# Kernel optimization log

Hardware: AMD Instinct MI355X
Metric: run time of the kernel (lower is better)

Reference implementation:

```python
import jax, jax.numpy as jnp
import numpy as np

B, V, S, T_IN, STEP, W, M = 4, 2, 256, 10, 5, 32, 16
NB = 6  # number of FNO2d blocks


def gelu(x):
    return jax.nn.gelu(x, approximate=False)  # torch F.gelu default = exact erf


def conv1(x, w, b):
    # 1x1x1 Conv3d: x (B,Cin,V,S,S), w (Cout,Cin), b (Cout,)
    return jnp.einsum('oc,bcvxy->bovxy', w, x) + b[None, :, None, None, None]


def spectral_conv(x, w1, w2):
    # x: (B,W,V,S,S) real; w1,w2: (W,W,V,M,M) complex64
    x_ft = jnp.fft.rfft2(x)  # (B,W,V,S,S//2+1) complex64
    o1 = jnp.einsum('bivxy,iovxy->bovxy', x_ft[..., :M, :M], w1)
    o2 = jnp.einsum('bivxy,iovxy->bovxy', x_ft[..., S - M:, :M], w2)
    F = S // 2 + 1
    out_ft = jnp.zeros((x.shape[0], W, V, S, F), jnp.complex64)
    out_ft = out_ft.at[..., :M, :M].set(o1).at[..., S - M:, :M].set(o2)
    return jnp.fft.irfft2(out_ft, s=(S, S))


def setup_inputs() -> dict:
    key = jax.random.key(0)
    ks = jax.random.split(key, 24)
    rn = lambda k, shp, s=0.05: jax.random.normal(k, shp, jnp.float32) * s
    sc = 1.0 / W  # torch init: scale * rand
    d = {}
    d['x'] = jax.random.normal(ks[0], (B, V, S, S, T_IN), jnp.float32)
    d['fc0_w'] = rn(ks[1], (T_IN + 2, W))
    d['fc0_b'] = rn(ks[2], (W,))
    d['w1r'] = jax.random.uniform(ks[3], (NB, W, W, V, M, M), jnp.float32) * sc
    d['w1i'] = jax.random.uniform(ks[4], (NB, W, W, V, M, M), jnp.float32) * sc
    d['w2r'] = jax.random.uniform(ks[5], (NB, W, W, V, M, M), jnp.float32) * sc
    d['w2i'] = jax.random.uniform(ks[6], (NB, W, W, V, M, M), jnp.float32) * sc
    d['mlp1_w'] = rn(ks[7], (NB, W, W))
    d['mlp1_b'] = rn(ks[8], (NB, W))
    d['mlp2_w'] = rn(ks[9], (NB, W, W))
    d['mlp2_b'] = rn(ks[10], (NB, W))
    d['ww'] = rn(ks[11], (NB, W, W))
    d['wb'] = rn(ks[12], (NB, W))
    d['bw'] = rn(ks[13], (NB, W, 2))
    d['bb'] = rn(ks[14], (NB, W))
    d['fc1_w'] = rn(ks[15], (W, 256))
    d['fc1_b'] = rn(ks[16], (256,))
    d['fc2_w'] = rn(ks[17], (256, STEP))
    d['fc2_b'] = rn(ks[18], (STEP,))
    return d


def reference(x, fc0_w, fc0_b, w1r, w1i, w2r, w2i, mlp1_w, mlp1_b, mlp2_w, mlp2_b,
              ww, wb, bw, bb, fc1_w, fc1_b, fc2_w, fc2_b):
    Bn = x.shape[0]
    gx = jnp.linspace(9.5, 10.5, S, dtype=jnp.float32)
    gy = jnp.linspace(-0.5, 0.5, S, dtype=jnp.float32)
    grid2 = jnp.stack([jnp.broadcast_to(gx[:, None], (S, S)),
                       jnp.broadcast_to(gy[None, :], (S, S))], 0)  # (2,S,S)
    grid = jnp.broadcast_to(grid2[None, :, None], (Bn, 2, V, S, S))  # (B,2,V,S,S)

    h = jnp.concatenate([x, jnp.transpose(grid, (0, 2, 3, 4, 1))], axis=-1)  # (B,V,S,S,T_IN+2)
    h = h @ fc0_w + fc0_b
    h = jnp.transpose(h, (0, 4, 1, 2, 3))  # (B,W,V,S,S)

    def block(i, h):
        x1 = spectral_conv(h, w1r[i] + 1j * w1i[i], w2r[i] + 1j * w2i[i])
        x1 = conv1(gelu(conv1(x1, mlp1_w[i], mlp1_b[i])), mlp2_w[i], mlp2_b[i])
        x2 = conv1(h, ww[i], wb[i])
        x3 = conv1(grid, bw[i], bb[i])
        return gelu(x1 + x2 + x3)

    x0 = block(0, h)
    h = block(1, x0)
    h = block(2, h) + x0
    x1s = block(3, h)
    h = block(4, x1s)
    h = block(5, h) + x1s

    h = jnp.transpose(h, (0, 2, 3, 4, 1))  # (B,V,S,S,W)
    h = gelu(h @ fc1_w + fc1_b)
    return h @ fc2_w + fc2_b  # (B,V,S,S,STEP)
```

## Files before the change

### kernel.cpp

```cpp
#include <hip/hip_runtime.h>

#define kB 4
#define kV 2
#define kS 256
#define kW 32
#define kM 16
#define kNB 6
#define kTIN 10
#define kSTEP 5

#define NPLANE 65536
#define NBWV   (kB*kW*kV)
#define BIGN   (kB*kW*kV*NPLANE)
#define CHS    (kV*NPLANE)

#define OFF_BIG0 0
#define OFF_BIG1 16777216
#define OFF_BIG2 33554432
#define OFF_FXR  52428800
#define OFF_FXI  52559872
#define OFF_GR   52690944
#define OFF_GI   52822016
#define OFF_TIC  52969472
#define OFF_TIS  52977664
#define OFF_IYC  52985856
#define OFF_IYS  52989952
#define OFF_WHI  52994048
#define OFF_WLO  52998144
#define OFF_YAH  53002240
#define OFF_YAL  53006336
#define OFF_XBH  53010432
#define OFF_XBL  53022720
#define OFF_M2H  53035008
#define OFF_M2L  53038080
#define OFF_WWH  53041152
#define OFF_WWL  53044224

typedef short bf16x8 __attribute__((ext_vector_type(8)));
typedef float f32x4 __attribute__((ext_vector_type(4)));

__device__ __forceinline__ unsigned short bf16_rne(float f){
    union { float f; unsigned int u; } x; x.f = f;
    unsigned int u = x.u + 0x7fffu + ((x.u>>16)&1u);
    return (unsigned short)(u>>16);
}
__device__ __forceinline__ float bf16_tof(unsigned short h){
    union { unsigned int u; float f; } x; x.u = ((unsigned int)h)<<16;
    return x.f;
}

__device__ __forceinline__ float gelu_f(float x){
    float z = fabsf(x) * 0.70710678118654752f;
    float t = __builtin_amdgcn_rcpf(1.0f + 0.3275911f*z);
    float poly = t*(0.254829592f + t*(-0.284496736f + t*(1.421413741f + t*(-1.453152027f + t*1.061405429f))));
    float e = __expf(-z*z);
    float erf_abs = 1.0f - poly*e;
    float ph = (x >= 0.0f) ? (1.0f + erf_abs) : (1.0f - erf_abs);
    return 0.5f * x * ph;
}

__global__ void k_tables(float* ws, const float* __restrict__ fc1w,
                         const float* __restrict__ m2w, const float* __restrict__ wwv){
    const double PI = 3.14159265358979323846;
    int t = blockIdx.x*256 + threadIdx.x;
    if (t < 8192){
        int j2 = t>>8, x2 = t&255;
        int kx2 = (j2<16) ? j2 : (224+j2);
        int p2 = (kx2*x2)&255;
        double a2 = (double)p2*(PI/128.0);
        ws[OFF_TIC+t] = (float)cos(a2);
        ws[OFF_TIS+t] = (float)sin(a2);
    }
    if (t < 4096){
        int k = t>>8, y = t&255;
        int p = (k*y)&255;
        double a = (double)p*(PI/128.0);
        float sc = 1.0f/65536.0f;
        ws[OFF_IYC+t] = (k==0 ? 1.0f : 2.0f*(float)cos(a))*sc;
        ws[OFF_IYS+t] = (k==0 ? 0.0f : -2.0f*(float)sin(a))*sc;
    }
    if (t < 1024){
        int nt = t>>6, l = t&63;
        int o = nt*16 + (l&15), c0 = (l>>4)*8;
        unsigned int hw[4], lw[4];
        #pragma unroll
        for (int e2=0; e2<4; e2++){
            float f0 = fc1w[(c0+2*e2  )*256 + o];
            float f1 = fc1w[(c0+2*e2+1)*256 + o];
            unsigned short h0 = bf16_rne(f0), h1 = bf16_rne(f1);
            unsigned short l0 = bf16_rne(f0 - bf16_tof(h0));
            unsigned short l1 = bf16_rne(f1 - bf16_tof(h1));
            hw[e2] = (unsigned int)h0 | ((unsigned int)h1<<16);
            lw[e2] = (unsigned int)l0 | ((unsigned int)l1<<16);
        }
        unsigned int* whi = (unsigned int*)(ws+OFF_WHI);
        unsigned int* wlo = (unsigned int*)(ws+OFF_WLO);
        #pragma unroll
        for (int e2=0; e2<4; e2++){
            whi[t*4+e2] = hw[e2];
            wlo[t*4+e2] = lw[e2];
        }
    }
    if (t < 1024){
        int mt = t>>9, kt = (t>>6)&7, l = t&63;
        int ky = l&15;
        unsigned int* yah = (unsigned int*)(ws+OFF_YAH);
        unsigned int* yal = (unsigned int*)(ws+OFF_YAL);
        #pragma unroll
        for (int e2=0; e2<4; e2++){
            int y0 = kt*32 + (l>>4)*8 + 2*e2;
            double a0 = (double)((ky*y0)&255)*(PI/128.0);
            double a1 = (double)((ky*(y0+1))&255)*(PI/128.0);
            float v0 = (mt==0) ? (float)cos(a0) : -(float)sin(a0);
            float v1 = (mt==0) ? (float)cos(a1) : -(float)sin(a1);
            unsigned short h0 = bf16_rne(v0), h1 = bf16_rne(v1);
            unsigned short s0 = bf16_rne(v0 - bf16_tof(h0));
            unsigned short s1 = bf16_rne(v1 - bf16_tof(h1));
            yah[t*4+e2] = (unsigned int)h0 | ((unsigned int)h1<<16);
            yal[t*4+e2] = (unsigned int)s0 | ((unsigned int)s1<<16);
        }
    }
    if (t < 3072){
        int tab = t>>10, jh = (t>>9)&1, kt = (t>>6)&7, l = t&63;
        int j = jh*16 + (l&15);
        int kx = (j<16) ? j : (224+j);
        unsigned int* xbh = (unsigned int*)(ws+OFF_XBH);
        unsigned int* xbl = (unsigned int*)(ws+OFF_XBL);
        #pragma unroll
        for (int e2=0; e2<4; e2++){
            int x0 = kt*32 + (l>>4)*8 + 2*e2;
            double a0 = (double)((kx*x0)&255)*(PI/128.0);
            double a1 = (double)((kx*(x0+1))&255)*(PI/128.0);
            float v0, v1;
            if (tab==0){ v0=(float)cos(a0); v1=(float)cos(a1); }
            else if (tab==1){ v0=-(float)sin(a0); v1=-(float)sin(a1); }
            else { v0=(float)sin(a0); v1=(float)sin(a1); }
            unsigned short h0 = bf16_rne(v0), h1 = bf16_rne(v1);
            unsigned short s0 = bf16_rne(v0 - bf16_tof(h0));
            unsigned short s1 = bf16_rne(v1 - bf16_tof(h1));
            xbh[t*4+e2] = (unsigned int)h0 | ((unsigned int)h1<<16);
            xbl[t*4+e2] = (unsigned int)s0 | ((unsigned int)s1<<16);
        }
    }
    if (t < 768){
        int blk = t>>7, rem = t&127, mt = rem>>6, l = rem&63;
        int o = mt*16 + (l&15), c0 = (l>>4)*8;
        const float* src = m2w + blk*1024;
        unsigned int* mh = (unsigned int*)(ws+OFF_M2H);
        unsigned int* ml = (unsigned int*)(ws+OFF_M2L);
        #pragma unroll
        for (int e2=0; e2<4; e2++){
            float f0 = src[o*32 + c0+2*e2];
            float f1 = src[o*32 + c0+2*e2+1];
            unsigned short h0 = bf16_rne(f0), h1 = bf16_rne(f1);
            unsigned short s0 = bf16_rne(f0 - bf16_tof(h0));
            unsigned short s1 = bf16_rne(f1 - bf16_tof(h1));
            mh[t*4+e2] = (unsigned int)h0 | ((unsigned int)h1<<16);
            ml[t*4+e2] = (unsigned int)s0 | ((unsigned int)s1<<16);
        }
    }
    if (t >= 768 && t < 1536){
        int t2 = t - 768;
        int blk = t2>>7, rem = t2&127, mt = rem>>6, l = rem&63;
        int o = mt*16 + (l&15), c0 = (l>>4)*8;
        const float* src = wwv + blk*1024;
        unsigned int* mh = (unsigned int*)(ws+OFF_WWH);
        unsigned int* ml = (unsigned int*)(ws+OFF_WWL);
        #pragma unroll
        for (int e2=0; e2<4; e2++){
            float f0 = src[o*32 + c0+2*e2];
            float f1 = src[o*32 + c0+2*e2+1];
            unsigned short h0 = bf16_rne(f0), h1 = bf16_rne(f1);
            unsigned short s0 = bf16_rne(f0 - bf16_tof(h0));
            unsigned short s1 = bf16_rne(f1 - bf16_tof(h1));
            mh[t2*4+e2] = (unsigned int)h0 | ((unsigned int)h1<<16);
            ml[t2*4+e2] = (unsigned int)s0 | ((unsigned int)s1<<16);
        }
    }
}

__global__ void k_fc0(const float* __restrict__ x, const float* __restrict__ w,
                      const float* __restrict__ bias, float* __restrict__ h0){
    int plane = blockIdx.x>>8, xr = blockIdx.x&255, y = threadIdx.x;
    int xy = xr*256+y;
    long p = (long)plane*NPLANE + xy;
    float f[12];
    #pragma unroll
    for (int i=0;i<10;i++) f[i]=x[p*10+i];
    f[10] = 9.5f + xr*(1.0f/255.0f);
    f[11] = -0.5f + y*(1.0f/255.0f);
    float acc[32];
    #pragma unroll
    for (int o=0;o<32;o++) acc[o]=bias[o];
    #pragma unroll
    for (int c=0;c<12;c++){
        float fv=f[c];
        #pragma unroll
        for (int o=0;o<32;o++) acc[o]+=fv*w[c*32+o];
    }
    int b=plane>>1, v=plane&1;
    int base = b*(kW*CHS) + v*NPLANE + xy;
    #pragma unroll
    for (int o=0;o<32;o++) h0[base + o*CHS]=acc[o];
}

__global__ __launch_bounds__(512) void k_fwdfft(const float* __restrict__ h,
        const unsigned int* __restrict__ yah, const unsigned int* __restrict__ yal,
        const unsigned int* __restrict__ xbh, const unsigned int* __restrict__ xbl,
        float* __restrict__ fxr, float* __restrict__ fxi){
    __shared__ float fyrl[16*260], fyil[16*260];
    int bwv = blockIdx.x;
    int tid = threadIdx.x;
    int wv = tid>>6, l = tid&63;

    for (int half=0; half<2; ++half){
        int nt = wv*2 + half;
        int x = nt*16 + (l&15);
        int klo = (l>>4)*8;
        const float* hp = h + bwv*NPLANE + x*256 + klo;
        f32x4 accR = {0.f,0.f,0.f,0.f}, accI = {0.f,0.f,0.f,0.f};
        for (int kt=0; kt<8; ++kt){
            float4 b0 = *reinterpret_cast<const float4*>(hp + kt*32);
            float4 b1 = *reinterpret_cast<const float4*>(hp + kt*32 + 4);
            float bv[8] = {b0.x,b0.y,b0.z,b0.w,b1.x,b1.y,b1.z,b1.w};
            bf16x8 bh, bl;
            #pragma unroll
            for (int e=0;e<8;e++){
                unsigned short hb = bf16_rne(bv[e]);
                bh[e] = (short)hb;
                bl[e] = (short)bf16_rne(bv[e] - bf16_tof(hb));
            }
            uint4 a0h = *reinterpret_cast<const uint4*>(&yah[(kt*64+l)*4]);
            uint4 a0l = *reinterpret_cast<const uint4*>(&yal[(kt*64+l)*4]);
            uint4 a1h = *reinterpret_cast<const uint4*>(&yah[(512 + kt*64 + l)*4]);
            uint4 a1l = *reinterpret_cast<const uint4*>(&yal[(512 + kt*64 + l)*4]);
            bf16x8 AH0 = __builtin_bit_cast(bf16x8, a0h);
            bf16x8 AL0 = __builtin_bit_cast(bf16x8, a0l);
            bf16x8 AH1 = __builtin_bit_cast(bf16x8, a1h);
            bf16x8 AL1 = __builtin_bit_cast(bf16x8, a1l);
            accR = __builtin_amdgcn_mfma_f32_16x16x32_bf16(AH0, bh, accR, 0,0,0);
            accR = __builtin_amdgcn_mfma_f32_16x16x32_bf16(AH0, bl, accR, 0,0,0);
            accR = __builtin_amdgcn_mfma_f32_16x16x32_bf16(AL0, bh, accR, 0,0,0);
            accI = __builtin_amdgcn_mfma_f32_16x16x32_bf16(AH1, bh, accI, 0,0,0);
            accI = __builtin_amdgcn_mfma_f32_16x16x32_bf16(AH1, bl, accI, 0,0,0);
            accI = __builtin_amdgcn_mfma_f32_16x16x32_bf16(AL1, bh, accI, 0,0,0);
        }
        int ky0 = (l>>4)*4;
        #pragma unroll
        for (int r=0;r<4;r++){
            fyrl[(ky0+r)*260 + x] = accR[r];
            fyil[(ky0+r)*260 + x] = accI[r];
        }
    }
    __syncthreads();

    if (wv < 2){
        int jh = wv;
        const float* ar = fyrl + (l&15)*260 + (l>>4)*8;
        const float* ai = fyil + (l&15)*260 + (l>>4)*8;
        f32x4 accR = {0.f,0.f,0.f,0.f}, accI = {0.f,0.f,0.f,0.f};
        for (int kt=0; kt<8; ++kt){
            float4 r0 = *reinterpret_cast<const float4*>(ar + kt*32);
            float4 r1 = *reinterpret_cast<const float4*>(ar + kt*32 + 4);
            float4 i0 = *reinterpret_cast<const float4*>(ai + kt*32);
            float4 i1 = *reinterpret_cast<const float4*>(ai + kt*32 + 4);
            float rv[8] = {r0.x,r0.y,r0.z,r0.w,r1.x,r1.y,r1.z,r1.w};
            float iv[8] = {i0.x,i0.y,i0.z,i0.w,i1.x,i1.y,i1.z,i1.w};
            bf16x8 Rh, Rl, Ih, Il;
            #pragma unroll
            for (int e=0;e<8;e++){
                unsigned short hb = bf16_rne(rv[e]);
                Rh[e] = (short)hb;
                Rl[e] = (short)bf16_rne(rv[e] - bf16_tof(hb));
                unsigned short hb2 = bf16_rne(iv[e]);
                Ih[e] = (short)hb2;
                Il[e] = (short)bf16_rne(iv[e] - bf16_tof(hb2));
            }
            int fb = (jh*512 + kt*64 + l)*4;
            uint4 ch = *reinterpret_cast<const uint4*>(&xbh[fb]);
            uint4 cl = *reinterpret_cast<const uint4*>(&xbl[fb]);
            uint4 sh = *reinterpret_cast<const uint4*>(&xbh[fb + 4096]);
            uint4 sl = *reinterpret_cast<const uint4*>(&xbl[fb + 4096]);
            uint4 ph = *reinterpret_cast<const uint4*>(&xbh[fb + 8192]);
            uint4 pl = *reinterpret_cast<const uint4*>(&xbl[fb + 8192]);
            bf16x8 CH = __builtin_bit_cast(bf16x8, ch);
            bf16x8 CL = __builtin_bit_cast(bf16x8, cl);
            bf16x8 SH = __builtin_bit_cast(bf16x8, sh);
            bf16x8 SL = __builtin_bit_cast(bf16x8, sl);
            bf16x8 PH = __builtin_bit_cast(bf16x8, ph);
            bf16x8 PL = __builtin_bit_cast(bf16x8, pl);
            accR = __builtin_amdgcn_mfma_f32_16x16x32_bf16(Rh, CH, accR, 0,0,0);
            accR = __builtin_amdgcn_mfma_f32_16x16x32_bf16(Rh, CL, accR, 0,0,0);
            accR = __builtin_amdgcn_mfma_f32_16x16x32_bf16(Rl, CH, accR, 0,0,0);
            accR = __builtin_amdgcn_mfma_f32_16x16x32_bf16(Ih, PH, accR, 0,0,0);
            accR = __builtin_amdgcn_mfma_f32_16x16x32_bf16(Ih, PL, accR, 0,0,0);
            accR = __builtin_amdgcn_mfma_f32_16x16x32_bf16(Il, PH, accR, 0,0,0);
            accI = __builtin_amdgcn_mfma_f32_16x16x32_bf16(Rh, SH, accI, 0,0,0);
            accI = __builtin_amdgcn_mfma_f32_16x16x32_bf16(Rh, SL, accI, 0,0,0);
            accI = __builtin_amdgcn_mfma_f32_16x16x32_bf16(Rl, SH, accI, 0,0,0);
            accI = __builtin_amdgcn_mfma_f32_16x16x32_bf16(Ih, CH, accI, 0,0,0);
            accI = __builtin_amdgcn_mfma_f32_16x16x32_bf16(Ih, CL, accI, 0,0,0);
            accI = __builtin_amdgcn_mfma_f32_16x16x32_bf16(Il, CH, accI, 0,0,0);
        }
        int ob = bwv*512 + jh*16 + (l&15);
        int ky0 = (l>>4)*4;
        #pragma unroll
        for (int r=0;r<4;r++){
            fxr[ob + (ky0+r)*32] = accR[r];
            fxi[ob + (ky0+r)*32] = accI[r];
        }
    }
}

__global__ void k_modemix(const float* __restrict__ fxr, const float* __restrict__ fxi,
                          const float* __restrict__ w1r_, const float* __restrict__ w1i_,
                          const float* __restrict__ w2r_, const float* __restrict__ w2i_,
                          const float* __restrict__ m1, float* __restrict__ g2r, float* __restrict__ g2i){
    __shared__ float glr[32*17], gli[32*17];
    int blk = blockIdx.x;
    int jh = blk&1, ky = (blk>>1)&15, v = (blk>>5)&1, b = blk>>6;
    int o = threadIdx.x>>4, jl = threadIdx.x&15;
    int j = jh*16 + jl;
    int kxi = (j<16) ? j : (j-16);
    const float* wr_ = (j<16) ? w1r_ : w2r_;
    const float* wi_ = (j<16) ? w1i_ : w2i_;
    int wbase = (o*kV + v)*256 + kxi*16 + ky;
    int fbase = (b*kW*kV + v)*512 + ky*32 + j;
    float re=0.f, im=0.f;
    #pragma unroll 8
    for (int i=0;i<32;i++){
        float fr=fxr[fbase+i*1024], fi=fxi[fbase+i*1024];
        float wr=wr_[wbase+i*16384], wi=wi_[wbase+i*16384];
        re += fr*wr - fi*wi;
        im += fr*wi + fi*wr;
    }
    glr[o*17+jl]=re; gli[o*17+jl]=im;
    __syncthreads();
    float r2=0.f, i2=0.f;
    #pragma unroll 8
    for (int i=0;i<32;i++){
        float m = m1[o*32+i];
        r2 += m*glr[i*17+jl];
        i2 += m*gli[i*17+jl];
    }
    int gid = ((b*kW + o)*kV + v)*512 + ky*32 + j;
    g2r[gid]=r2; g2i[gid]=i2;
}

__global__ void k_invpoint(const float* __restrict__ g2r, const float* __restrict__ g2i,
                           const float* __restrict__ xic, const float* __restrict__ xis,
                           const float* __restrict__ iyc, const float* __restrict__ iys,
                           const float* __restrict__ b1,
                           const float* h, const float* res, float* out,
                           const unsigned int* __restrict__ m2h, const unsigned int* __restrict__ m2l,
                           const unsigned int* __restrict__ wwh, const unsigned int* __restrict__ wwl,
                           const float* __restrict__ b2,
                           const float* __restrict__ wb_, const float* __restrict__ bw_,
                           const float* __restrict__ bb_){
    __shared__ float frl[16*36], fil[16*36];
    __shared__ float tl[32*260];
    __shared__ float cinit[32], bwy_[32];
    int tid = threadIdx.x;
    int blk = blockIdx.x;
    int b = blk>>9, v = (blk>>8)&1, xr = blk&255;
    float gx = 9.5f + xr*(1.0f/255.0f);
    if (tid < 32){
        cinit[tid] = b2[tid] + wb_[tid] + bb_[tid] + bw_[tid*2]*gx;
        bwy_[tid] = bw_[tid*2+1];
    }

    #pragma unroll
    for (int pp=0; pp<2; pp++){
        int p = tid + pp*256;
        int o = p>>4, k = p&15;
        const float* gr_ = g2r + (((b*kW + o)*kV + v)<<9) + k*32;
        const float* gi_ = g2i + (((b*kW + o)*kV + v)<<9) + k*32;
        float re=0.f, im=0.f;
        #pragma unroll 8
        for (int j=0;j<32;j++){
            float grv=gr_[j], giv=gi_[j];
            float c=xic[j*256+xr], s=xis[j*256+xr];
            re += grv*c - giv*s;
            im += grv*s + giv*c;
        }
        frl[k*36+o]=re; fil[k*36+o]=im;
    }
    __syncthreads();

    {
        int og = tid&7, yg = tid>>3;
        int o0 = og*4, y0 = yg*8;
        float acc[4][8];
        #pragma unroll
        for (int oo=0;oo<4;oo++){
            float bb1 = b1[o0+oo];
            #pragma unroll
            for (int yy=0;yy<8;yy++) acc[oo][yy]=bb1;
        }
        #pragma unroll 4
        for (int k=0;k<16;k++){
            float4 yc0 = *reinterpret_cast<const float4*>(&iyc[k*256+y0]);
            float4 yc1 = *reinterpret_cast<const float4*>(&iyc[k*256+y0+4]);
            float4 ys0 = *reinterpret_cast<const float4*>(&iys[k*256+y0]);
            float4 ys1 = *reinterpret_cast<const float4*>(&iys[k*256+y0+4]);
            float4 fr4 = *reinterpret_cast<const float4*>(&frl[k*36+o0]);
            float4 fi4 = *reinterpret_cast<const float4*>(&fil[k*36+o0]);
            float frv[4]={fr4.x,fr4.y,fr4.z,fr4.w};
            float fiv[4]={fi4.x,fi4.y,fi4.z,fi4.w};
            #pragma unroll
            for (int oo=0;oo<4;oo++){
                acc[oo][0] += frv[oo]*yc0.x + fiv[oo]*ys0.x;
                acc[oo][1] += frv[oo]*yc0.y + fiv[oo]*ys0.y;
                acc[oo][2] += frv[oo]*yc0.z + fiv[oo]*ys0.z;
                acc[oo][3] += frv[oo]*yc0.w + fiv[oo]*ys0.w;
                acc[oo][4] += frv[oo]*yc1.x + fiv[oo]*ys1.x;
                acc[oo][5] += frv[oo]*yc1.y + fiv[oo]*ys1.y;
                acc[oo][6] += frv[oo]*yc1.z + fiv[oo]*ys1.z;
                acc[oo][7] += frv[oo]*yc1.w + fiv[oo]*ys1.w;
            }
        }
        #pragma unroll
        for (int oo=0;oo<4;oo++){
            float4 w0, w1;
            w0.x = gelu_f(acc[oo][0]); w0.y = gelu_f(acc[oo][1]);
            w0.z = gelu_f(acc[oo][2]); w0.w = gelu_f(acc[oo][3]);
            w1.x = gelu_f(acc[oo][4]); w1.y = gelu_f(acc[oo][5]);
            w1.z = gelu_f(acc[oo][6]); w1.w = gelu_f(acc[oo][7]);
            *reinterpret_cast<float4*>(&tl[(o0+oo)*260 + y0])   = w0;
            *reinterpret_cast<float4*>(&tl[(o0+oo)*260 + y0+4]) = w1;
        }
    }
    __syncthreads();

    int wv = tid>>6, l = tid&63;
    int lm = l&15, lg = l>>4;
    int pb = b*(kW*CHS) + v*NPLANE + xr*256;
    bf16x8 M2Hf[2], M2Lf[2], WWHf[2], WWLf[2];
    #pragma unroll
    for (int mt=0; mt<2; ++mt){
        M2Hf[mt] = __builtin_bit_cast(bf16x8, *reinterpret_cast<const uint4*>(&m2h[(mt*64+l)*4]));
        M2Lf[mt] = __builtin_bit_cast(bf16x8, *reinterpret_cast<const uint4*>(&m2l[(mt*64+l)*4]));
        WWHf[mt] = __builtin_bit_cast(bf16x8, *reinterpret_cast<const uint4*>(&wwh[(mt*64+l)*4]));
        WWLf[mt] = __builtin_bit_cast(bf16x8, *reinterpret_cast<const uint4*>(&wwl[(mt*64+l)*4]));
    }
    for (int nt=0; nt<4; ++nt){
        int y0 = wv*64 + nt*16;
        int yy = y0 + lm;
        float gyv = -0.5f + yy*(1.0f/255.0f);
        bf16x8 th, tlw, hh, hlw;
        #pragma unroll
        for (int e=0;e<8;e++){
            float tvv = tl[(lg*8+e)*260 + yy];
            unsigned short tb = bf16_rne(tvv);
            th[e] = (short)tb;
            tlw[e] = (short)bf16_rne(tvv - bf16_tof(tb));
            float hvv = h[pb + (lg*8+e)*CHS + yy];
            unsigned short hb = bf16_rne(hvv);
            hh[e] = (short)hb;
            hlw[e] = (short)bf16_rne(hvv - bf16_tof(hb));
        }
        for (int mt=0; mt<2; ++mt){
            f32x4 d = {0.f,0.f,0.f,0.f};
            d = __builtin_amdgcn_mfma_f32_16x16x32_bf16(M2Hf[mt], th,  d, 0,0,0);
            d = __builtin_amdgcn_mfma_f32_16x16x32_bf16(M2Hf[mt], tlw, d, 0,0,0);
            d = __builtin_amdgcn_mfma_f32_16x16x32_bf16(M2Lf[mt], th,  d, 0,0,0);
            d = __builtin_amdgcn_mfma_f32_16x16x32_bf16(WWHf[mt], hh,  d, 0,0,0);
            d = __builtin_amdgcn_mfma_f32_16x16x32_bf16(WWHf[mt], hlw, d, 0,0,0);
            d = __builtin_amdgcn_mfma_f32_16x16x32_bf16(WWLf[mt], hh,  d, 0,0,0);
            #pragma unroll
            for (int r=0;r<4;r++){
                int o = mt*16 + lg*4 + r;
                float val = gelu_f(d[r] + cinit[o] + bwy_[o]*gyv);
                int addr = pb + o*CHS + yy;
                if (res) val += res[addr];
                out[addr] = val;
            }
        }
    }
}

__global__ __launch_bounds__(256) void k_head(const float* __restrict__ h,
        const unsigned int* __restrict__ whi, const unsigned int* __restrict__ wlo,
        const float* __restrict__ fc1b, const float* __restrict__ fc2w,
        const float* __restrict__ fc2b, float* __restrict__ out){
    __shared__ float hl[32*257];
    int tid = threadIdx.x;
    int plane = blockIdx.x>>8, xr = blockIdx.x&255;
    int b = plane>>1, v = plane&1;
    const float* hp = h + b*(kW*CHS) + v*NPLANE + xr*256;
    #pragma unroll 8
    for (int c=0;c<32;c++) hl[c*257 + tid] = hp[c*CHS + tid];
    __syncthreads();

    int wv = tid>>6, l = tid&63;
    int lm = l&15, lg = l>>4;
    float f2b[5];
    #pragma unroll
    for (int j=0;j<5;j++) f2b[j] = fc2b[j];

    for (int mt=0; mt<4; ++mt){
        int pxl = wv*64 + mt*16 + lm;
        bf16x8 ah;
        #pragma unroll
        for (int e=0;e<8;e++){
            float a = hl[(lg*8+e)*257 + pxl];
            ah[e] = (short)bf16_rne(a);
        }
        float fj[4][5];
        #pragma unroll
        for (int r=0;r<4;r++)
            #pragma unroll
            for (int j=0;j<5;j++) fj[r][j]=0.f;
        for (int q=0; q<4; ++q){
            #pragma unroll
            for (int ntq=0; ntq<4; ntq++){
                int nt = q*4 + ntq;
                uint4 rh = *reinterpret_cast<const uint4*>(&whi[(nt*64+l)*4]);
                uint4 rl = *reinterpret_cast<const uint4*>(&wlo[(nt*64+l)*4]);
                bf16x8 BH = __builtin_bit_cast(bf16x8, rh);
                bf16x8 BL = __builtin_bit_cast(bf16x8, rl);
                f32x4 d = {0.f,0.f,0.f,0.f};
                d = __builtin_amdgcn_mfma_f32_16x16x32_bf16(ah, BH, d, 0,0,0);
                d = __builtin_amdgcn_mfma_f32_16x16x32_bf16(ah, BL, d, 0,0,0);
                int o = nt*16 + lm;
                float b1  = fc1b[o];
                float w20 = fc2w[o*5+0], w21 = fc2w[o*5+1], w22 = fc2w[o*5+2];
                float w23 = fc2w[o*5+3], w24 = fc2w[o*5+4];
                #pragma unroll
                for (int r=0;r<4;r++){
                    float u = gelu_f(d[r] + b1);
                    fj[r][0] += u*w20; fj[r][1] += u*w21; fj[r][2] += u*w22;
                    fj[r][3] += u*w23; fj[r][4] += u*w24;
                }
            }
        }
        #pragma unroll
        for (int m=1; m<16; m<<=1){
            #pragma unroll
            for (int r=0;r<4;r++){
                #pragma unroll
                for (int j=0;j<5;j++) fj[r][j] += __shfl_xor(fj[r][j], m, 64);
            }
        }
        if (lm == 0){
            int prow = blockIdx.x*256 + wv*64 + mt*16 + lg*4;
            #pragma unroll
            for (int r=0;r<4;r++){
                long ob = (long)(prow+r)*5;
                #pragma unroll
                for (int j=0;j<5;j++) out[ob+j] = fj[r][j] + f2b[j];
            }
        }
    }
}

extern "C" void kernel_launch(void* const* d_in, const int* in_sizes, int n_in,
                              void* d_out, int out_size, void* d_ws, size_t ws_size,
                              hipStream_t stream){
    const float* x    =(const float*)d_in[0];
    const float* fc0w =(const float*)d_in[1];
    const float* fc0b =(const float*)d_in[2];
    const float* w1r  =(const float*)d_in[3];
    const float* w1i  =(const float*)d_in[4];
    const float* w2r  =(const float*)d_in[5];
    const float* w2i  =(const float*)d_in[6];
    const float* m1w  =(const float*)d_in[7];
    const float* m1b  =(const float*)d_in[8];
    const float* m2w  =(const float*)d_in[9];
    const float* m2b  =(const float*)d_in[10];
    const float* ww   =(const float*)d_in[11];
    const float* wb   =(const float*)d_in[12];
    const float* bw   =(const float*)d_in[13];
    const float* bb   =(const float*)d_in[14];
    const float* fc1w =(const float*)d_in[15];
    const float* fc1b =(const float*)d_in[16];
    const float* fc2w =(const float*)d_in[17];
    const float* fc2b =(const float*)d_in[18];

    float* ws = (float*)d_ws;
    float* big[3] = {ws+OFF_BIG0, ws+OFF_BIG1, ws+OFF_BIG2};
    float* fxr = ws+OFF_FXR; float* fxi = ws+OFF_FXI;
    float* gr  = ws+OFF_GR;  float* gi  = ws+OFF_GI;

    k_tables<<<32,256,0,stream>>>(ws, fc1w, m2w, ww);
    k_fc0<<<2048,256,0,stream>>>(x, fc0w, fc0b, big[0]);

    const int s_in [6] = {0,0,2,2,2,0};
    const int s_out[6] = {0,2,2,2,0,0};
    const int s_res[6] = {-1,-1,0,-1,-1,2};

    for (int blk=0; blk<6; ++blk){
        float* in   = big[s_in[blk]];
        float* outb = big[s_out[blk]];
        const float* resp = (s_res[blk] < 0) ? nullptr : big[s_res[blk]];
        k_fwdfft<<<256,512,0,stream>>>(in,
            (const unsigned int*)(ws+OFF_YAH), (const unsigned int*)(ws+OFF_YAL),
            (const unsigned int*)(ws+OFF_XBH), (const unsigned int*)(ws+OFF_XBL),
            fxr, fxi);
        k_modemix<<<256,512,0,stream>>>(fxr, fxi,
            w1r+blk*524288, w1i+blk*524288, w2r+blk*524288, w2i+blk*524288,
            m1w+blk*1024, gr, gi);
        k_invpoint<<<2048,256,0,stream>>>(gr, gi, ws+OFF_TIC, ws+OFF_TIS,
            ws+OFF_IYC, ws+OFF_IYS, m1b+blk*32,
            in, resp, outb,
            (const unsigned int*)(ws+OFF_M2H) + blk*512,
            (const unsigned int*)(ws+OFF_M2L) + blk*512,
            (const unsigned int*)(ws+OFF_WWH) + blk*512,
            (const unsigned int*)(ws+OFF_WWL) + blk*512,
            m2b+blk*32, wb+blk*32, bw+blk*64, bb+blk*32);
    }
    k_head<<<2048,256,0,stream>>>(big[0],
        (const unsigned int*)(ws+OFF_WHI), (const unsigned int*)(ws+OFF_WLO),
        fc1b, fc2w, fc2b, (float*)d_out);
}
```

Measured before the change: 1.001 ms.

## Repack spectral weights into coalesced layout for mode-mixing kernel

Adds a kernel that transposes the complex spectral weights of all six blocks into a layout where the output channel is contiguous, reusing the unused BIG1 workspace region. The mode-mixing kernel then maps threads so that consecutive lanes read consecutive weights. It stages its results through shared memory so the global stores keep their original layout. The aim is to replace strided, uncoalesced weight reads with coalesced ones, at the cost of a one-time repack pass over about 50 MB of weights on each call.

```diff
diff --git a/kernel.cpp b/kernel.cpp
--- a/kernel.cpp
+++ b/kernel.cpp
@@ -15,7 +15,8 @@
 #define CHS    (kV*NPLANE)
 
 #define OFF_BIG0 0
-#define OFF_BIG1 16777216
+#define OFF_WPR  16777216
+#define OFF_WPI  23068672
 #define OFF_BIG2 33554432
 #define OFF_FXR  52428800
 #define OFF_FXI  52559872
@@ -176,6 +177,30 @@
             mh[t2*4+e2] = (unsigned int)h0 | ((unsigned int)h1<<16);
             ml[t2*4+e2] = (unsigned int)s0 | ((unsigned int)s1<<16);
         }
+    }
+}
+
+__global__ void k_wpack(const float* __restrict__ w1r, const float* __restrict__ w1i,
+                        const float* __restrict__ w2r, const float* __restrict__ w2i,
+                        float* __restrict__ wpr, float* __restrict__ wpi){
+    __shared__ float lds[32*272];
+    int bid = blockIdx.x;
+    int blk = bid>>8, rem = bid&255;
+    int i = rem>>3, v = (rem>>2)&1, part = (rem>>1)&1, jh = rem&1;
+    const float* src0 = (part==0) ? (jh==0 ? w1r : w2r) : (jh==0 ? w1i : w2i);
+    const float* src = src0 + blk*524288;
+    int tid = threadIdx.x;
+    for (int o=0;o<32;o++){
+        lds[o*272 + (tid>>4)*17 + (tid&15)] = src[((i*32+o)*2+v)*256 + tid];
+    }
+    __syncthreads();
+    float* dst = ((part==0) ? wpr : wpi);
+    int o = tid&31, grp = tid>>5;
+    for (int p=0;p<32;p++){
+        int pair = p*8 + grp;
+        int ky = pair>>4, kxi = pair&15;
+        int j = jh*16 + kxi;
+        dst[((((blk*2+v)*16+ky)*32 + j)*32 + i)*32 + o] = lds[o*272 + kxi*17 + ky];
     }
 }
 
@@ -313,38 +338,39 @@
 }
 
 __global__ void k_modemix(const float* __restrict__ fxr, const float* __restrict__ fxi,
-                          const float* __restrict__ w1r_, const float* __restrict__ w1i_,
-                          const float* __restrict__ w2r_, const float* __restrict__ w2i_,
+                          const float* __restrict__ wpr, const float* __restrict__ wpi,
                           const float* __restrict__ m1, float* __restrict__ g2r, float* __restrict__ g2i){
-    __shared__ float glr[32*17], gli[32*17];
+    __shared__ float glr[32*17], gli[32*17], g2rl[32*17], g2il[32*17];
     int blk = blockIdx.x;
     int jh = blk&1, ky = (blk>>1)&15, v = (blk>>5)&1, b = blk>>6;
-    int o = threadIdx.x>>4, jl = threadIdx.x&15;
-    int j = jh*16 + jl;
-    int kxi = (j<16) ? j : (j-16);
-    const float* wr_ = (j<16) ? w1r_ : w2r_;
-    const float* wi_ = (j<16) ? w1i_ : w2i_;
-    int wbase = (o*kV + v)*256 + kxi*16 + ky;
+    int o = threadIdx.x&31, jg = threadIdx.x>>5;
+    int j = jh*16 + jg;
+    const float* wr = wpr + ((((v*16+ky)*32 + j)*32)<<5) + o;
+    const float* wi = wpi + ((((v*16+ky)*32 + j)*32)<<5) + o;
     int fbase = (b*kW*kV + v)*512 + ky*32 + j;
     float re=0.f, im=0.f;
     #pragma unroll 8
     for (int i=0;i<32;i++){
         float fr=fxr[fbase+i*1024], fi=fxi[fbase+i*1024];
-        float wr=wr_[wbase+i*16384], wi=wi_[wbase+i*16384];
-        re += fr*wr - fi*wi;
-        im += fr*wi + fi*wr;
-    }
-    glr[o*17+jl]=re; gli[o*17+jl]=im;
+        float wrv=wr[i*32], wiv=wi[i*32];
+        re += fr*wrv - fi*wiv;
+        im += fr*wiv + fi*wrv;
+    }
+    glr[o*17+jg]=re; gli[o*17+jg]=im;
     __syncthreads();
     float r2=0.f, i2=0.f;
     #pragma unroll 8
     for (int i=0;i<32;i++){
         float m = m1[o*32+i];
-        r2 += m*glr[i*17+jl];
-        i2 += m*gli[i*17+jl];
-    }
-    int gid = ((b*kW + o)*kV + v)*512 + ky*32 + j;
-    g2r[gid]=r2; g2i[gid]=i2;
+        r2 += m*glr[i*17+jg];
+        i2 += m*gli[i*17+jg];
+    }
+    g2rl[o*17+jg]=r2; g2il[o*17+jg]=i2;
+    __syncthreads();
+    int o2 = threadIdx.x>>4, jl2 = threadIdx.x&15;
+    int gid = ((b*kW + o2)*kV + v)*512 + ky*32 + jh*16 + jl2;
+    g2r[gid] = g2rl[o2*17+jl2];
+    g2i[gid] = g2il[o2*17+jl2];
 }
 
 __global__ void k_invpoint(const float* __restrict__ g2r, const float* __restrict__ g2i,
@@ -578,11 +604,13 @@
     const float* fc2b =(const float*)d_in[18];
 
     float* ws = (float*)d_ws;
-    float* big[3] = {ws+OFF_BIG0, ws+OFF_BIG1, ws+OFF_BIG2};
+    float* big[3] = {ws+OFF_BIG0, nullptr, ws+OFF_BIG2};
     float* fxr = ws+OFF_FXR; float* fxi = ws+OFF_FXI;
     float* gr  = ws+OFF_GR;  float* gi  = ws+OFF_GI;
+    float* wpr = ws+OFF_WPR; float* wpi = ws+OFF_WPI;
 
     k_tables<<<32,256,0,stream>>>(ws, fc1w, m2w, ww);
+    k_wpack<<<1536,256,0,stream>>>(w1r, w1i, w2r, w2i, wpr, wpi);
     k_fc0<<<2048,256,0,stream>>>(x, fc0w, fc0b, big[0]);
 
     const int s_in [6] = {0,0,2,2,2,0};
@@ -598,7 +626,7 @@
             (const unsigned int*)(ws+OFF_XBH), (const unsigned int*)(ws+OFF_XBL),
             fxr, fxi);
         k_modemix<<<256,512,0,stream>>>(fxr, fxi,
-            w1r+blk*524288, w1i+blk*524288, w2r+blk*524288, w2i+blk*524288,
+            wpr + blk*1048576, wpi + blk*1048576,
             m1w+blk*1024, gr, gi);
         k_invpoint<<<2048,256,0,stream>>>(gr, gi, ws+OFF_TIC, ws+OFF_TIS,
             ws+OFF_IYC, ws+OFF_IYS, m1b+blk*32,
```

New measurement: 935.9 us. 6.5% less time.
